# Kernel optimization log

Hardware: AMD Instinct MI355X
Metric: run time of the kernel (lower is better)

## Reference

```python
import jax, jax.numpy as jnp
import numpy as np

IDEAL_C1_C1 = 6.0
MIN_C1_DIST = 3.4
L = 4096
W_BOND, W_CLASH, W_PAIR = 1.0, 2.0, 0.5


def setup_inputs() -> dict:
    key = jax.random.key(0)
    k1, k2 = jax.random.split(key)
    # Spread coordinates so distances span a realistic range (some clashes, some far)
    coords = jax.random.normal(k1, (L, 3), dtype=jnp.float32) * 20.0
    u = jax.random.uniform(k2, (L, L), dtype=jnp.float32)
    contact_map = (u < 0.01).astype(jnp.float32)
    return {"coords": coords, "contact_map": contact_map}


def reference(coords, contact_map):
    Ln = coords.shape[0]
    # ---- bond energy: harmonic on consecutive C1'-C1' distances ----
    diff = coords[1:] - coords[:-1]                      # [L-1, 3]
    bond_dist = jnp.linalg.norm(diff, axis=-1)
    e_bond = jnp.mean((bond_dist - IDEAL_C1_C1) ** 2)

    # ---- all-pairs distances (matches per-pair norm + 1e-8 of the original) ----
    d = jnp.sqrt(jnp.sum((coords[:, None, :] - coords[None, :, :]) ** 2, axis=-1)) + 1e-8  # [L, L]

    idx = jnp.arange(Ln)
    sep = idx[None, :] - idx[:, None]                    # j - i

    # ---- clash energy: soft-sphere over pairs with j >= i + 3 ----
    clash_mask = sep >= 3
    clash = jax.nn.relu(MIN_C1_DIST - d)
    e_clash = jnp.sum(jnp.where(clash_mask, clash ** 2, 0.0)) / Ln

    # ---- pair energy: attract contacts (|i-j| >= 3) toward 1.5 * ideal dist ----
    # NOTE: divisor counts ALL contact pairs (including |i-j| < 3 ones), as original
    target_dist = IDEAL_C1_C1 * 1.5
    contact = contact_map > 0.5
    n_pairs = jnp.sum(contact)
    pmask = contact & (jnp.abs(sep) >= 3)
    e_pair = jnp.sum(jnp.where(pmask, (d - target_dist) ** 2, 0.0)) / jnp.maximum(n_pairs, 1)

    total = W_BOND * e_bond + W_CLASH * e_clash + W_PAIR * e_pair
    return total.reshape(1)  # original returns shape-(1,) tensor
```

## Files before the change

kernel.cpp:

```cpp
#include <hip/hip_runtime.h>

#define LSEQ 4096
#define ROWS 2
#define NB (LSEQ / ROWS)
#define NT 256

#define IDEAL 6.0f
#define MIN_DIST 3.4f
#define TARGET 9.0f
#define W_BOND 1.0f
#define W_CLASH 2.0f
#define W_PAIR 0.5f


__global__ __launch_bounds__(NT) void er_pair(
        const float* __restrict__ coords,
        const float* __restrict__ cmap,
        float4* __restrict__ ws) {
    const int t = threadIdx.x;
    const int b = blockIdx.x;
    const int i0 = b * ROWS, i1 = i0 + 1;

    const float4* cp4 = (const float4*)coords;
    const float4* crow0 = (const float4*)(cmap + (size_t)i0 * LSEQ);
    const float4* crow1 = (const float4*)(cmap + (size_t)i1 * LSEQ);

    float4 M00 = crow0[t +   0], M01 = crow0[t + 256],
           M02 = crow0[t + 512], M03 = crow0[t + 768];
    float4 M10 = crow1[t +   0], M11 = crow1[t + 256],
           M12 = crow1[t + 512], M13 = crow1[t + 768];

    float4 A = cp4[3 * t + 0];
    float4 B = cp4[3 * t + 1];
    float4 C = cp4[3 * t + 2];

    const float xi0 = coords[3 * i0 + 0], yi0 = coords[3 * i0 + 1], zi0 = coords[3 * i0 + 2];
    const float xi1 = coords[3 * i1 + 0], yi1 = coords[3 * i1 + 1], zi1 = coords[3 * i1 + 2];

    float cl0 = 0.0f, cl1 = 0.0f;
    float pr0 = 0.0f, pr1 = 0.0f;
    float ct0 = 0.0f, ct1 = 0.0f;

#define COMP_TILE(K, A_, B_, C_, M0, M1)                                      \
    do {                                                                      \
        const float xs[4] = {A_.x, A_.w, B_.z, C_.y};                         \
        const float ys[4] = {A_.y, B_.x, B_.w, C_.z};                         \
        const float zs[4] = {A_.z, B_.y, C_.x, C_.w};                         \
        const float cv0[4] = {M0.x, M0.y, M0.z, M0.w};                        \
        const float cv1[4] = {M1.x, M1.y, M1.z, M1.w};                        \
        const int jbase = 4 * t + 1024 * (K);                                 \
        _Pragma("unroll")                                                     \
        for (int q = 0; q < 4; ++q) {                                         \
            const int sep0 = jbase + q - i0;             \
            {                                                      \
                const float dx = xi0 - xs[q];                                 \
                const float dy = yi0 - ys[q];                                 \
                const float dz = zi0 - zs[q];                                 \
                const float d2 = fmaf(dx, dx, fmaf(dy, dy, dz * dz));         \
                const float d = __builtin_amdgcn_sqrtf(d2);                   \
                float cl = fmaxf(MIN_DIST - d, 0.0f);                         \
                cl = (sep0 >= 3) ? cl : 0.0f;                                 \
                cl0 = fmaf(cl, cl, cl0);                                      \
                const float pdm = ((unsigned int)(sep0 + 2) > 4u)             \
                                      ? (d - TARGET) : 0.0f;                  \
                pr0 = fmaf(cv0[q] * pdm, pdm, pr0);                           \
                ct0 += cv0[q];                                                \
            }                                                                 \
            {                                                      \
                const float dx = xi1 - xs[q];                                 \
                const float dy = yi1 - ys[q];                                 \
                const float dz = zi1 - zs[q];                                 \
                const float d2 = fmaf(dx, dx, fmaf(dy, dy, dz * dz));         \
                const float d = __builtin_amdgcn_sqrtf(d2);                   \
                float cl = fmaxf(MIN_DIST - d, 0.0f);                         \
                cl = (sep0 >= 4) ? cl : 0.0f;                                 \
                cl1 = fmaf(cl, cl, cl1);                                      \
                const float pdm = ((unsigned int)(sep0 + 1) > 4u)             \
                                      ? (d - TARGET) : 0.0f;                  \
                pr1 = fmaf(cv1[q] * pdm, pdm, pr1);                           \
                ct1 += cv1[q];                                                \
            }                                                                 \
        }                                                                     \
    } while (0)

    float4 An, Bn, Cn;

    An = cp4[3 * t + 768 + 0]; Bn = cp4[3 * t + 768 + 1]; Cn = cp4[3 * t + 768 + 2];
    COMP_TILE(0, A, B, C, M00, M10);
    A = An; B = Bn; C = Cn;

    An = cp4[3 * t + 1536 + 0]; Bn = cp4[3 * t + 1536 + 1]; Cn = cp4[3 * t + 1536 + 2];
    COMP_TILE(1, A, B, C, M01, M11);
    A = An; B = Bn; C = Cn;

    An = cp4[3 * t + 2304 + 0]; Bn = cp4[3 * t + 2304 + 1]; Cn = cp4[3 * t + 2304 + 2];
    COMP_TILE(2, A, B, C, M02, M12);
    A = An; B = Bn; C = Cn;

    COMP_TILE(3, A, B, C, M03, M13);

#undef COMP_TILE

    float clash_acc = cl0 + cl1;
    float pair_acc = pr0 + pr1;
    float cnt_acc = ct0 + ct1;

#pragma unroll
    for (int off = 32; off > 0; off >>= 1) {
        clash_acc += __shfl_down(clash_acc, off);
        pair_acc  += __shfl_down(pair_acc, off);
        cnt_acc   += __shfl_down(cnt_acc, off);
    }
    __shared__ float s_clash[NT / 64], s_pair[NT / 64], s_cnt[NT / 64];
    const int wave = t >> 6;
    const int lane = t & 63;
    if (lane == 0) { s_clash[wave] = clash_acc; s_pair[wave] = pair_acc; s_cnt[wave] = cnt_acc; }
    __syncthreads();
    if (t == 0) {
        float cs = 0.0f, ps = 0.0f, ns = 0.0f;
#pragma unroll
        for (int w = 0; w < NT / 64; ++w) { cs += s_clash[w]; ps += s_pair[w]; ns += s_cnt[w]; }
        ws[b] = make_float4(cs, ps, ns, 0.0f);
    }
}

__global__ __launch_bounds__(NT) void er_finalize(
        const float* __restrict__ coords,
        const float4* __restrict__ ws,
        float* __restrict__ out) {
    const int t = threadIdx.x;
    float cs = 0.0f, ps = 0.0f, ns = 0.0f;
    for (int idx = t; idx < NB; idx += NT) {
        const float4 v = ws[idx];
        cs += v.x; ps += v.y; ns += v.z;
    }
    float bacc = 0.0f;
    for (int s = t; s < LSEQ - 1; s += NT) {
        const float dx = coords[3 * (s + 1) + 0] - coords[3 * s + 0];
        const float dy = coords[3 * (s + 1) + 1] - coords[3 * s + 1];
        const float dz = coords[3 * (s + 1) + 2] - coords[3 * s + 2];
        const float d = __builtin_amdgcn_sqrtf(fmaf(dx, dx, fmaf(dy, dy, dz * dz)));
        const float e = d - IDEAL;
        bacc += e * e;
    }
#pragma unroll
    for (int off = 32; off > 0; off >>= 1) {
        cs += __shfl_down(cs, off);
        ps += __shfl_down(ps, off);
        ns += __shfl_down(ns, off);
        bacc += __shfl_down(bacc, off);
    }
    __shared__ float sc[NT / 64], sp[NT / 64], sn[NT / 64], sb[NT / 64];
    const int wave = t >> 6;
    const int lane = t & 63;
    if (lane == 0) { sc[wave] = cs; sp[wave] = ps; sn[wave] = ns; sb[wave] = bacc; }
    __syncthreads();
    if (t == 0) {
        float tc = 0.0f, tp = 0.0f, tn = 0.0f, tb = 0.0f;
#pragma unroll
        for (int w = 0; w < NT / 64; ++w) { tc += sc[w]; tp += sp[w]; tn += sn[w]; tb += sb[w]; }
        const float e_bond = tb / (float)(LSEQ - 1);
        const float e_clash = tc / (float)LSEQ;
        const float e_pair = tp / fmaxf(tn, 1.0f);
        out[0] = W_BOND * e_bond + W_CLASH * e_clash + W_PAIR * e_pair;
    }
}

extern "C" void kernel_launch(void* const* d_in, const int* in_sizes, int n_in,
                              void* d_out, int out_size, void* d_ws, size_t ws_size,
                              hipStream_t stream) {
    const float* coords = (const float*)d_in[0];
    const float* cmap   = (const float*)d_in[1];
    float4* ws = (float4*)d_ws;
    float* out = (float*)d_out;

    hipLaunchKernelGGL(er_pair, dim3(NB), dim3(NT), 0, stream, coords, cmap, ws);
    hipLaunchKernelGGL(er_finalize, dim3(1), dim3(NT), 0, stream, coords, ws, out);
}
```

Measured before the change: 102.6 us.

## Use 1024-thread blocks covering full rows, each handling 8 strided rows

The pair kernel now launches 512 blocks of 1024 threads. Each thread holds one fixed 4-column slice of coordinates in registers and processes 8 rows (4 interleaved row pairs strided across the sequence), so the per-tile coordinate reloads disappear. Contact-map rows are double-buffered so the next pair is loaded while the current one is computed. This cuts coordinate traffic and partial-result count, in exchange for fewer, larger blocks and more registers per thread, which may reduce occupancy and latency hiding on what is a bandwidth-bound read of the 64 MB contact map.

```diff
diff --git a/kernel.cpp b/kernel.cpp
--- a/kernel.cpp
+++ b/kernel.cpp
@@ -1,9 +1,10 @@
 #include <hip/hip_runtime.h>
 
 #define LSEQ 4096
-#define ROWS 2
-#define NB (LSEQ / ROWS)
-#define NT 256
+#define NT   1024
+#define IT   4
+#define NBLK (LSEQ / (2 * IT))
+#define FNT  256
 
 #define IDEAL 6.0f
 #define MIN_DIST 3.4f
@@ -19,43 +20,49 @@
         float4* __restrict__ ws) {
     const int t = threadIdx.x;
     const int b = blockIdx.x;
-    const int i0 = b * ROWS, i1 = i0 + 1;
 
     const float4* cp4 = (const float4*)coords;
-    const float4* crow0 = (const float4*)(cmap + (size_t)i0 * LSEQ);
-    const float4* crow1 = (const float4*)(cmap + (size_t)i1 * LSEQ);
+    const float4* cm4 = (const float4*)cmap;
 
-    float4 M00 = crow0[t +   0], M01 = crow0[t + 256],
-           M02 = crow0[t + 512], M03 = crow0[t + 768];
-    float4 M10 = crow1[t +   0], M11 = crow1[t + 256],
-           M12 = crow1[t + 512], M13 = crow1[t + 768];
+    const float4 A = cp4[3 * t + 0];
+    const float4 B = cp4[3 * t + 1];
+    const float4 C = cp4[3 * t + 2];
 
-    float4 A = cp4[3 * t + 0];
-    float4 B = cp4[3 * t + 1];
-    float4 C = cp4[3 * t + 2];
-
-    const float xi0 = coords[3 * i0 + 0], yi0 = coords[3 * i0 + 1], zi0 = coords[3 * i0 + 2];
-    const float xi1 = coords[3 * i1 + 0], yi1 = coords[3 * i1 + 1], zi1 = coords[3 * i1 + 2];
+    float xi0[IT], yi0[IT], zi0[IT], xi1[IT], yi1[IT], zi1[IT];
+#pragma unroll
+    for (int k = 0; k < IT; ++k) {
+        const int i0 = 2 * (b + k * NBLK);
+        xi0[k] = coords[3 * i0 + 0];
+        yi0[k] = coords[3 * i0 + 1];
+        zi0[k] = coords[3 * i0 + 2];
+        xi1[k] = coords[3 * i0 + 3];
+        yi1[k] = coords[3 * i0 + 4];
+        zi1[k] = coords[3 * i0 + 5];
+    }
 
     float cl0 = 0.0f, cl1 = 0.0f;
     float pr0 = 0.0f, pr1 = 0.0f;
     float ct0 = 0.0f, ct1 = 0.0f;
 
-#define COMP_TILE(K, A_, B_, C_, M0, M1)                                      \
+    const int j0 = 4 * t;
+
+#define ROWIDX(k, r) ((size_t)(2 * (b + (k) * NBLK) + (r)) * (LSEQ / 4) + t)
+
+#define COMP(kk, M0, M1)                                                      \
     do {                                                                      \
-        const float xs[4] = {A_.x, A_.w, B_.z, C_.y};                         \
-        const float ys[4] = {A_.y, B_.x, B_.w, C_.z};                         \
-        const float zs[4] = {A_.z, B_.y, C_.x, C_.w};                         \
+        const int i0 = 2 * (b + (kk) * NBLK);                                 \
+        const float xs[4] = {A.x, A.w, B.z, C.y};                             \
+        const float ys[4] = {A.y, B.x, B.w, C.z};                             \
+        const float zs[4] = {A.z, B.y, C.x, C.w};                             \
         const float cv0[4] = {M0.x, M0.y, M0.z, M0.w};                        \
         const float cv1[4] = {M1.x, M1.y, M1.z, M1.w};                        \
-        const int jbase = 4 * t + 1024 * (K);                                 \
         _Pragma("unroll")                                                     \
         for (int q = 0; q < 4; ++q) {                                         \
-            const int sep0 = jbase + q - i0;             \
+            const int sep0 = j0 + q - i0;                \
             {                                                      \
-                const float dx = xi0 - xs[q];                                 \
-                const float dy = yi0 - ys[q];                                 \
-                const float dz = zi0 - zs[q];                                 \
+                const float dx = xi0[kk] - xs[q];                             \
+                const float dy = yi0[kk] - ys[q];                             \
+                const float dz = zi0[kk] - zs[q];                             \
                 const float d2 = fmaf(dx, dx, fmaf(dy, dy, dz * dz));         \
                 const float d = __builtin_amdgcn_sqrtf(d2);                   \
                 float cl = fmaxf(MIN_DIST - d, 0.0f);                         \
@@ -67,9 +74,9 @@
                 ct0 += cv0[q];                                                \
             }                                                                 \
             {                                                      \
-                const float dx = xi1 - xs[q];                                 \
-                const float dy = yi1 - ys[q];                                 \
-                const float dz = zi1 - zs[q];                                 \
+                const float dx = xi1[kk] - xs[q];                             \
+                const float dy = yi1[kk] - ys[q];                             \
+                const float dz = zi1[kk] - zs[q];                             \
                 const float d2 = fmaf(dx, dx, fmaf(dy, dy, dz * dz));         \
                 const float d = __builtin_amdgcn_sqrtf(d2);                   \
                 float cl = fmaxf(MIN_DIST - d, 0.0f);                         \
@@ -83,23 +90,18 @@
         }                                                                     \
     } while (0)
 
-    float4 An, Bn, Cn;
+    float4 mA0 = cm4[ROWIDX(0, 0)], mA1 = cm4[ROWIDX(0, 1)];
+    float4 mB0 = cm4[ROWIDX(1, 0)], mB1 = cm4[ROWIDX(1, 1)];
 
-    An = cp4[3 * t + 768 + 0]; Bn = cp4[3 * t + 768 + 1]; Cn = cp4[3 * t + 768 + 2];
-    COMP_TILE(0, A, B, C, M00, M10);
-    A = An; B = Bn; C = Cn;
+    COMP(0, mA0, mA1);
+    mA0 = cm4[ROWIDX(2, 0)]; mA1 = cm4[ROWIDX(2, 1)];
+    COMP(1, mB0, mB1);
+    mB0 = cm4[ROWIDX(3, 0)]; mB1 = cm4[ROWIDX(3, 1)];
+    COMP(2, mA0, mA1);
+    COMP(3, mB0, mB1);
 
-    An = cp4[3 * t + 1536 + 0]; Bn = cp4[3 * t + 1536 + 1]; Cn = cp4[3 * t + 1536 + 2];
-    COMP_TILE(1, A, B, C, M01, M11);
-    A = An; B = Bn; C = Cn;
-
-    An = cp4[3 * t + 2304 + 0]; Bn = cp4[3 * t + 2304 + 1]; Cn = cp4[3 * t + 2304 + 2];
-    COMP_TILE(2, A, B, C, M02, M12);
-    A = An; B = Bn; C = Cn;
-
-    COMP_TILE(3, A, B, C, M03, M13);
-
-#undef COMP_TILE
+#undef COMP
+#undef ROWIDX
 
     float clash_acc = cl0 + cl1;
     float pair_acc = pr0 + pr1;
@@ -124,18 +126,18 @@
     }
 }
 
-__global__ __launch_bounds__(NT) void er_finalize(
+__global__ __launch_bounds__(FNT) void er_finalize(
         const float* __restrict__ coords,
         const float4* __restrict__ ws,
         float* __restrict__ out) {
     const int t = threadIdx.x;
     float cs = 0.0f, ps = 0.0f, ns = 0.0f;
-    for (int idx = t; idx < NB; idx += NT) {
+    for (int idx = t; idx < NBLK; idx += FNT) {
         const float4 v = ws[idx];
         cs += v.x; ps += v.y; ns += v.z;
     }
     float bacc = 0.0f;
-    for (int s = t; s < LSEQ - 1; s += NT) {
+    for (int s = t; s < LSEQ - 1; s += FNT) {
         const float dx = coords[3 * (s + 1) + 0] - coords[3 * s + 0];
         const float dy = coords[3 * (s + 1) + 1] - coords[3 * s + 1];
         const float dz = coords[3 * (s + 1) + 2] - coords[3 * s + 2];
@@ -150,7 +152,7 @@
         ns += __shfl_down(ns, off);
         bacc += __shfl_down(bacc, off);
     }
-    __shared__ float sc[NT / 64], sp[NT / 64], sn[NT / 64], sb[NT / 64];
+    __shared__ float sc[FNT / 64], sp[FNT / 64], sn[FNT / 64], sb[FNT / 64];
     const int wave = t >> 6;
     const int lane = t & 63;
     if (lane == 0) { sc[wave] = cs; sp[wave] = ps; sn[wave] = ns; sb[wave] = bacc; }
@@ -158,7 +160,7 @@
     if (t == 0) {
         float tc = 0.0f, tp = 0.0f, tn = 0.0f, tb = 0.0f;
 #pragma unroll
-        for (int w = 0; w < NT / 64; ++w) { tc += sc[w]; tp += sp[w]; tn += sn[w]; tb += sb[w]; }
+        for (int w = 0; w < FNT / 64; ++w) { tc += sc[w]; tp += sp[w]; tn += sn[w]; tb += sb[w]; }
         const float e_bond = tb / (float)(LSEQ - 1);
         const float e_clash = tc / (float)LSEQ;
         const float e_pair = tp / fmaxf(tn, 1.0f);
@@ -174,6 +176,6 @@
     float4* ws = (float4*)d_ws;
     float* out = (float*)d_out;
 
-    hipLaunchKernelGGL(er_pair, dim3(NB), dim3(NT), 0, stream, coords, cmap, ws);
-    hipLaunchKernelGGL(er_finalize, dim3(1), dim3(NT), 0, stream, coords, ws, out);
+    hipLaunchKernelGGL(er_pair, dim3(NBLK), dim3(NT), 0, stream, coords, cmap, ws);
+    hipLaunchKernelGGL(er_finalize, dim3(1), dim3(FNT), 0, stream, coords, ws, out);
 }
```

Result: no change. 100.7 us (-1.9%).
